# Kernel optimization log

Measured on AMD Instinct MI355X. Metric: run time of the kernel, lower is better.

## Reference

```python
import jax, jax.numpy as jnp
import numpy as np

EPS = 1e-8  # torch F.cosine_similarity default eps


def setup_inputs() -> dict:
    key = jax.random.key(0)
    k1, k2, k3 = jax.random.split(key, 3)
    B, S, D, O, W = 256, 10, 4096, 4096, 5
    x = jax.random.normal(k1, (B, S, D), dtype=jnp.float32)
    # Conv1d params: weight [out, in, kernel], bias [out]
    conv_w = jax.random.normal(k2, (O, D, W), dtype=jnp.float32) * (1.0 / np.sqrt(D * W))
    conv_b = jax.random.normal(k3, (O,), dtype=jnp.float32) * 0.01
    return {"x": x, "conv_w": conv_w, "conv_b": conv_b}


def reference(x, conv_w, conv_b):
    B, S, D = x.shape
    # central frame: original code uses index S//2 + 1 (faithful off-by-one)
    central = x[:, S // 2 + 1, :]  # [B, D]
    dots = jnp.einsum('bsd,bd->bs', x, central)  # [B, S]
    xn = jnp.maximum(jnp.linalg.norm(x, axis=-1), EPS)      # [B, S]
    cn = jnp.maximum(jnp.linalg.norm(central, axis=-1), EPS)  # [B]
    cos = dots / (xn * cn[:, None])  # [B, S]
    # original multiplies by RAW (unnormalized) cosine weights
    xw = x * cos[:, :, None]  # [B, S, D]
    # conv1d over time: [B, D, S] -> [B, O, S-W+1]
    y = jax.lax.conv_general_dilated(
        jnp.transpose(xw, (0, 2, 1)), conv_w,
        window_strides=(1,), padding='VALID',
        dimension_numbers=('NCH', 'OIH', 'NCH'))
    y = y + conv_b[None, :, None]
    return jnp.mean(y, axis=-1)  # [B, O]
```

## Files before the change

kernel.cpp:

```cpp
#include <hip/hip_runtime.h>


#define BDIM 256
#define SEQ 10
#define DDIM 4096
#define ODIM 4096
#define WDIM 5
#define GK 20480
#define SPLITS 8
#define KSPLIT (GK / SPLITS)
#define BK 64
#define KITERS (KSPLIT / BK)

typedef __bf16 bf16x8 __attribute__((ext_vector_type(8)));
typedef float f32x4 __attribute__((ext_vector_type(4)));

__device__ __forceinline__ unsigned short f2bf(float f) {
    union { float f; unsigned v; } c; c.f = f;
    unsigned r = c.v + 0x7FFFu + ((c.v >> 16) & 1u);
    return (unsigned short)(r >> 16);
}
__device__ __forceinline__ void async16(void* lds, const void* g) {
    __builtin_amdgcn_global_load_lds(
        (const __attribute__((address_space(1))) void*)g,
        (__attribute__((address_space(3))) void*)lds, 16, 0, 0);
}

#define VMWAIT(n) asm volatile("s_waitcnt vmcnt(" #n ")" ::: "memory")
#define LGKM0()   asm volatile("s_waitcnt lgkmcnt(0)" ::: "memory")
#define SBAR()    __builtin_amdgcn_s_barrier()
#define SCHED0()  __builtin_amdgcn_sched_barrier(0)

__global__ __launch_bounds__(256) void cosp_kernel(const float* __restrict__ x,
                                                   unsigned short* __restrict__ P)
{
    const int b = blockIdx.x;
    const int tid = threadIdx.x;
    const float* xb = x + (size_t)b * SEQ * DDIM;

    float dot[SEQ], sq[SEQ];
#pragma unroll
    for (int s = 0; s < SEQ; ++s) { dot[s] = 0.f; sq[s] = 0.f; }

    for (int base = 0; base < DDIM; base += 1024) {
        const int d = base + tid * 4;
        const f32x4 c4 = *(const f32x4*)(xb + 6 * DDIM + d);
#pragma unroll
        for (int s = 0; s < SEQ; ++s) {
            const f32x4 v4 = *(const f32x4*)(xb + s * DDIM + d);
            dot[s] += v4[0] * c4[0] + v4[1] * c4[1] + v4[2] * c4[2] + v4[3] * c4[3];
            sq[s]  += v4[0] * v4[0] + v4[1] * v4[1] + v4[2] * v4[2] + v4[3] * v4[3];
        }
    }
#pragma unroll
    for (int s = 0; s < SEQ; ++s) {
#pragma unroll
        for (int off = 32; off > 0; off >>= 1) {
            dot[s] += __shfl_down(dot[s], off, 64);
            sq[s]  += __shfl_down(sq[s], off, 64);
        }
    }
    __shared__ float red[4][2 * SEQ];
    __shared__ float cs[SEQ];
    const int wave = tid >> 6, lane = tid & 63;
    if (lane == 0) {
#pragma unroll
        for (int s = 0; s < SEQ; ++s) { red[wave][s] = dot[s]; red[wave][SEQ + s] = sq[s]; }
    }
    __syncthreads();
    if (tid == 0) {
        const float S6 = red[0][SEQ + 6] + red[1][SEQ + 6] + red[2][SEQ + 6] + red[3][SEQ + 6];
        const float cn = fmaxf(sqrtf(S6), 1e-8f);
#pragma unroll
        for (int s = 0; s < SEQ; ++s) {
            const float Dv = red[0][s] + red[1][s] + red[2][s] + red[3][s];
            const float Sv = red[0][SEQ + s] + red[1][SEQ + s] + red[2][SEQ + s] + red[3][SEQ + s];
            cs[s] = Dv / (fmaxf(sqrtf(Sv), 1e-8f) * cn);
        }
    }
    __syncthreads();

    float csr[SEQ];
#pragma unroll
    for (int s = 0; s < SEQ; ++s) csr[s] = cs[s];

    for (int chunk = 3; chunk >= 0; --chunk) {
        const int d0 = chunk * 1024 + tid * 4;
        const float* xd = xb + d0;
        float sc[SEQ][4];
#pragma unroll
        for (int s = 0; s < SEQ; ++s) {
            const f32x4 v4 = *(const f32x4*)(xd + s * DDIM);
            sc[s][0] = v4[0] * csr[s]; sc[s][1] = v4[1] * csr[s];
            sc[s][2] = v4[2] * csr[s]; sc[s][3] = v4[3] * csr[s];
        }
        __attribute__((aligned(16))) unsigned short o[20];
#pragma unroll
        for (int w = 0; w < WDIM; ++w) {
#pragma unroll
            for (int j = 0; j < 4; ++j) {
                const float p = sc[w][j] + sc[w + 1][j] + sc[w + 2][j] +
                                sc[w + 3][j] + sc[w + 4][j] + sc[w + 5][j];
                o[j * WDIM + w] = f2bf(p);
            }
        }
        unsigned short* dst = P + ((size_t)b * DDIM + d0) * WDIM;
#pragma unroll
        for (int q = 0; q < 5; ++q)
            *(uint2*)(dst + q * 4) = *(const uint2*)(o + q * 4);
    }
}

__global__ __launch_bounds__(256, 2) void gemm_splitk_kernel(const unsigned short* __restrict__ A,
                                                             const float* __restrict__ W,
                                                             float* __restrict__ Cpart)
{
    const int bid = blockIdx.x;
    const int sp = bid & 7;
    const int nt = bid >> 3;
    const int tid = threadIdx.x;
    const int lane = tid & 63;
    const int wave = tid >> 6;

    __shared__ __align__(16) unsigned short lds_a[2][256 * BK];
    __shared__ __align__(16) unsigned short lds_w[2][64 * BK];

    f32x4 acc[4][4];
#pragma unroll
    for (int i = 0; i < 4; ++i)
#pragma unroll
        for (int j = 0; j < 4; ++j)
            acc[i][j] = (f32x4){0.f, 0.f, 0.f, 0.f};

    const int s_arow = tid >> 3;
    const int s_aoct = tid & 7;

    const int s_wrow = tid >> 2;
    const float* wsrc = W + ((size_t)(nt * 64 + s_wrow)) * GK + (tid & 3) * 16;
    const int wo0 = (((tid & 3) * 2)     ^ (s_wrow & 7)) * 8;
    const int wo1 = (((tid & 3) * 2 + 1) ^ (s_wrow & 7)) * 8;

    const int fm = lane & 15;
    const int fg = lane >> 4;
    int aoff[2][4], woff[2][4];
#pragma unroll
    for (int i = 0; i < 4; ++i) {
        const int ra = wave * 64 + i * 16 + fm;
        const int rw = i * 16 + fm;
#pragma unroll
        for (int kh = 0; kh < 2; ++kh) {
            aoff[kh][i] = ra * BK + (((kh * 4 + fg) ^ (ra & 7)) * 8);
            woff[kh][i] = rw * BK + (((kh * 4 + fg) ^ (rw & 7)) * 8);
        }
    }

#define STAGE_A(buf, kk)                                                        \
    _Pragma("unroll")                                                           \
    for (int q = 0; q < 8; ++q) {                                               \
        const int row_ = q * 32 + s_arow;                                       \
        const unsigned short* src_ =                                            \
            A + (size_t)row_ * GK + (kk) + ((s_aoct ^ (row_ & 7)) * 8);         \
        async16((char*)&lds_a[buf][0] + q * 4096 + tid * 16, src_);             \
    }

#define LOAD_W(R0, R1, R2, R3, kk)                                              \
    R0 = *(const f32x4*)(wsrc + (kk));                                          \
    R1 = *(const f32x4*)(wsrc + (kk) + 4);                                      \
    R2 = *(const f32x4*)(wsrc + (kk) + 8);                                      \
    R3 = *(const f32x4*)(wsrc + (kk) + 12);

#define WRITE_W(buf, R0, R1, R2, R3)                                            \
    {                                                                           \
        bf16x8 lo_, hi_;                                                        \
        _Pragma("unroll")                                                       \
        for (int e = 0; e < 4; ++e) {                                           \
            lo_[e] = (__bf16)R0[e]; lo_[4 + e] = (__bf16)R1[e];                 \
            hi_[e] = (__bf16)R2[e]; hi_[4 + e] = (__bf16)R3[e];                 \
        }                                                                       \
        *(bf16x8*)&lds_w[buf][s_wrow * BK + wo0] = lo_;                         \
        *(bf16x8*)&lds_w[buf][s_wrow * BK + wo1] = hi_;                         \
    }

#define COMPUTE(buf)                                                            \
    _Pragma("unroll")                                                           \
    for (int kh = 0; kh < 2; ++kh) {                                            \
        bf16x8 af[4], wf[4];                                                    \
        _Pragma("unroll")                                                       \
        for (int i = 0; i < 4; ++i) af[i] = *(const bf16x8*)&lds_a[buf][aoff[kh][i]]; \
        _Pragma("unroll")                                                       \
        for (int j = 0; j < 4; ++j) wf[j] = *(const bf16x8*)&lds_w[buf][woff[kh][j]]; \
        _Pragma("unroll")                                                       \
        for (int i = 0; i < 4; ++i)                                             \
            _Pragma("unroll")                                                   \
            for (int j = 0; j < 4; ++j)                                         \
                acc[i][j] = __builtin_amdgcn_mfma_f32_16x16x32_bf16(            \
                    af[i], wf[j], acc[i][j], 0, 0, 0);                          \
    }

    const int ksp = sp * KSPLIT;
    f32x4 wA0, wA1, wA2, wA3;
    f32x4 wB0, wB1, wB2, wB3;

    LOAD_W(wA0, wA1, wA2, wA3, ksp);
    STAGE_A(0, ksp);
    VMWAIT(8); SCHED0();
    WRITE_W(0, wA0, wA1, wA2, wA3);
    LOAD_W(wB0, wB1, wB2, wB3, ksp + BK);
    VMWAIT(4); SCHED0();
    LGKM0();
    SBAR(); SCHED0();

    int kbase = ksp;
    for (int tt = 0; tt < (KITERS - 2) / 2; ++tt) {
        SCHED0();
        STAGE_A(1, kbase + BK);
        LOAD_W(wA0, wA1, wA2, wA3, kbase + 2 * BK);
        VMWAIT(12); SCHED0();
        COMPUTE(0);
        WRITE_W(1, wB0, wB1, wB2, wB3);
        LGKM0();
        SBAR(); SCHED0();
        kbase += BK;
        STAGE_A(0, kbase + BK);
        LOAD_W(wB0, wB1, wB2, wB3, kbase + 2 * BK);
        VMWAIT(12); SCHED0();
        COMPUTE(1);
        WRITE_W(0, wA0, wA1, wA2, wA3);
        LGKM0();
        SBAR(); SCHED0();
        kbase += BK;
    }
    STAGE_A(1, kbase + BK);
    VMWAIT(8); SCHED0();
    COMPUTE(0);
    WRITE_W(1, wB0, wB1, wB2, wB3);
    LGKM0();
    SBAR(); SCHED0();
    VMWAIT(0); SCHED0();
    COMPUTE(1);

    float* Cp = Cpart + (size_t)sp * (BDIM * ODIM);
    const int mbase = wave * 64 + fg * 4;
    const int nbase = nt * 64 + fm;
#pragma unroll
    for (int i = 0; i < 4; ++i)
#pragma unroll
        for (int j = 0; j < 4; ++j) {
            const int n = nbase + j * 16;
#pragma unroll
            for (int r = 0; r < 4; ++r) {
                const int m = mbase + i * 16 + r;
                Cp[(size_t)m * ODIM + n] = acc[i][j][r];
            }
        }
#undef STAGE_A
#undef LOAD_W
#undef WRITE_W
#undef COMPUTE
}

__global__ __launch_bounds__(256) void reduce_kernel(const float* __restrict__ part,
                                                     const float* __restrict__ bias,
                                                     float* __restrict__ out)
{
    const int idx = (blockIdx.x * 256 + threadIdx.x) * 4;
    f32x4 s = (f32x4){0.f, 0.f, 0.f, 0.f};
#pragma unroll
    for (int sp = 0; sp < SPLITS; ++sp) {
        const f32x4 v = *(const f32x4*)(part + (size_t)sp * (BDIM * ODIM) + idx);
        s[0] += v[0]; s[1] += v[1]; s[2] += v[2]; s[3] += v[3];
    }
    const int n = idx & (ODIM - 1);
    const f32x4 b4 = *(const f32x4*)(bias + n);
    const float inv6 = 1.0f / 6.0f;
    f32x4 o;
#pragma unroll
    for (int e = 0; e < 4; ++e) o[e] = s[e] * inv6 + b4[e];
    *(f32x4*)(out + idx) = o;
}

extern "C" void kernel_launch(void* const* d_in, const int* in_sizes, int n_in,
                              void* d_out, int out_size, void* d_ws, size_t ws_size,
                              hipStream_t stream) {
    const float* x  = (const float*)d_in[0];
    const float* cw = (const float*)d_in[1];
    const float* cb = (const float*)d_in[2];
    float* out = (float*)d_out;

    char* ws = (char*)d_ws;
    unsigned short* P = (unsigned short*)(ws + 16384);
    float* parts = (float*)(ws + 16384 + (size_t)BDIM * GK * 2);

    hipLaunchKernelGGL(cosp_kernel,        dim3(256),  dim3(256), 0, stream, x, P);
    hipLaunchKernelGGL(gemm_splitk_kernel, dim3(512),  dim3(256), 0, stream, P, cw, parts);
    hipLaunchKernelGGL(reduce_kernel,      dim3(1024), dim3(256), 0, stream, parts, cb, out);
}
```

Before: 493.3 us.

## Narrow GEMM N-tile to 32, halve split-K count, and move W waits after compute

Shrinks each block's output tile from 256x64 to 256x32 and cuts the split-K factor from 8 to 4, so the block count stays the same but each block covers twice the K range. Partial-sum writes and the final reduction shrink accordingly. W loads now move 8 floats per thread, and the vmcnt waits sit after the MFMA compute so W loads overlap with math. The narrower tile means the A operand is re-streamed by twice as many N-tiles. Each block also gets less MFMA work per LDS read, which may hurt arithmetic intensity.

```diff
diff --git a/kernel.cpp b/kernel.cpp
--- a/kernel.cpp
+++ b/kernel.cpp
@@ -7,10 +7,11 @@
 #define ODIM 4096
 #define WDIM 5
 #define GK 20480
-#define SPLITS 8
+#define SPLITS 4
 #define KSPLIT (GK / SPLITS)
 #define BK 64
 #define KITERS (KSPLIT / BK)
+#define NT 32
 
 typedef __bf16 bf16x8 __attribute__((ext_vector_type(8)));
 typedef float f32x4 __attribute__((ext_vector_type(4)));
@@ -116,41 +117,43 @@
                                                              float* __restrict__ Cpart)
 {
     const int bid = blockIdx.x;
-    const int sp = bid & 7;
-    const int nt = bid >> 3;
+    const int sp = bid & 3;
+    const int nt = bid >> 2;
     const int tid = threadIdx.x;
     const int lane = tid & 63;
     const int wave = tid >> 6;
 
     __shared__ __align__(16) unsigned short lds_a[2][256 * BK];
-    __shared__ __align__(16) unsigned short lds_w[2][64 * BK];
-
-    f32x4 acc[4][4];
+    __shared__ __align__(16) unsigned short lds_w[2][NT * BK];
+
+    f32x4 acc[4][2];
 #pragma unroll
     for (int i = 0; i < 4; ++i)
 #pragma unroll
-        for (int j = 0; j < 4; ++j)
+        for (int j = 0; j < 2; ++j)
             acc[i][j] = (f32x4){0.f, 0.f, 0.f, 0.f};
 
     const int s_arow = tid >> 3;
     const int s_aoct = tid & 7;
 
-    const int s_wrow = tid >> 2;
-    const float* wsrc = W + ((size_t)(nt * 64 + s_wrow)) * GK + (tid & 3) * 16;
-    const int wo0 = (((tid & 3) * 2)     ^ (s_wrow & 7)) * 8;
-    const int wo1 = (((tid & 3) * 2 + 1) ^ (s_wrow & 7)) * 8;
+    const int s_wrow = tid >> 3;
+    const float* wsrc = W + ((size_t)(nt * NT + s_wrow)) * GK + (tid & 7) * 8;
+    const int wo0 = (((tid & 7)) ^ (s_wrow & 7)) * 8;
 
     const int fm = lane & 15;
     const int fg = lane >> 4;
-    int aoff[2][4], woff[2][4];
-#pragma unroll
-    for (int i = 0; i < 4; ++i) {
-        const int ra = wave * 64 + i * 16 + fm;
-        const int rw = i * 16 + fm;
-#pragma unroll
-        for (int kh = 0; kh < 2; ++kh) {
+    int aoff[2][4], woff[2][2];
+#pragma unroll
+    for (int kh = 0; kh < 2; ++kh) {
+#pragma unroll
+        for (int i = 0; i < 4; ++i) {
+            const int ra = wave * 64 + i * 16 + fm;
             aoff[kh][i] = ra * BK + (((kh * 4 + fg) ^ (ra & 7)) * 8);
-            woff[kh][i] = rw * BK + (((kh * 4 + fg) ^ (rw & 7)) * 8);
+        }
+#pragma unroll
+        for (int j = 0; j < 2; ++j) {
+            const int rw = j * 16 + fm;
+            woff[kh][j] = rw * BK + (((kh * 4 + fg) ^ (rw & 7)) * 8);
         }
     }
 
@@ -163,50 +166,44 @@
         async16((char*)&lds_a[buf][0] + q * 4096 + tid * 16, src_);             \
     }
 
-#define LOAD_W(R0, R1, R2, R3, kk)                                              \
+#define LOAD_W(R0, R1, kk)                                                      \
     R0 = *(const f32x4*)(wsrc + (kk));                                          \
-    R1 = *(const f32x4*)(wsrc + (kk) + 4);                                      \
-    R2 = *(const f32x4*)(wsrc + (kk) + 8);                                      \
-    R3 = *(const f32x4*)(wsrc + (kk) + 12);
-
-#define WRITE_W(buf, R0, R1, R2, R3)                                            \
+    R1 = *(const f32x4*)(wsrc + (kk) + 4);
+
+#define WRITE_W(buf, R0, R1)                                                    \
     {                                                                           \
-        bf16x8 lo_, hi_;                                                        \
-        _Pragma("unroll")                                                       \
-        for (int e = 0; e < 4; ++e) {                                           \
-            lo_[e] = (__bf16)R0[e]; lo_[4 + e] = (__bf16)R1[e];                 \
-            hi_[e] = (__bf16)R2[e]; hi_[4 + e] = (__bf16)R3[e];                 \
-        }                                                                       \
-        *(bf16x8*)&lds_w[buf][s_wrow * BK + wo0] = lo_;                         \
-        *(bf16x8*)&lds_w[buf][s_wrow * BK + wo1] = hi_;                         \
+        bf16x8 v_;                                                              \
+        _Pragma("unroll")                                                       \
+        for (int e = 0; e < 4; ++e) { v_[e] = (__bf16)R0[e]; v_[4 + e] = (__bf16)R1[e]; } \
+        *(bf16x8*)&lds_w[buf][s_wrow * BK + wo0] = v_;                          \
     }
 
 #define COMPUTE(buf)                                                            \
     _Pragma("unroll")                                                           \
     for (int kh = 0; kh < 2; ++kh) {                                            \
-        bf16x8 af[4], wf[4];                                                    \
+        bf16x8 af[4], wf[2];                                                    \
         _Pragma("unroll")                                                       \
         for (int i = 0; i < 4; ++i) af[i] = *(const bf16x8*)&lds_a[buf][aoff[kh][i]]; \
         _Pragma("unroll")                                                       \
-        for (int j = 0; j < 4; ++j) wf[j] = *(const bf16x8*)&lds_w[buf][woff[kh][j]]; \
+        for (int j = 0; j < 2; ++j) wf[j] = *(const bf16x8*)&lds_w[buf][woff[kh][j]]; \
         _Pragma("unroll")                                                       \
         for (int i = 0; i < 4; ++i)                                             \
             _Pragma("unroll")                                                   \
-            for (int j = 0; j < 4; ++j)                                         \
+            for (int j = 0; j < 2; ++j)                                         \
                 acc[i][j] = __builtin_amdgcn_mfma_f32_16x16x32_bf16(            \
                     af[i], wf[j], acc[i][j], 0, 0, 0);                          \
     }
 
     const int ksp = sp * KSPLIT;
-    f32x4 wA0, wA1, wA2, wA3;
-    f32x4 wB0, wB1, wB2, wB3;
-
-    LOAD_W(wA0, wA1, wA2, wA3, ksp);
+    f32x4 wA0, wA1;
+    f32x4 wB0, wB1;
+
+    LOAD_W(wA0, wA1, ksp);
     STAGE_A(0, ksp);
-    VMWAIT(8); SCHED0();
-    WRITE_W(0, wA0, wA1, wA2, wA3);
-    LOAD_W(wB0, wB1, wB2, wB3, ksp + BK);
-    VMWAIT(4); SCHED0();
+    LOAD_W(wB0, wB1, ksp + BK);
+    VMWAIT(10); SCHED0();
+    WRITE_W(0, wA0, wA1);
+    VMWAIT(2); SCHED0();
     LGKM0();
     SBAR(); SCHED0();
 
@@ -214,38 +211,40 @@
     for (int tt = 0; tt < (KITERS - 2) / 2; ++tt) {
         SCHED0();
         STAGE_A(1, kbase + BK);
-        LOAD_W(wA0, wA1, wA2, wA3, kbase + 2 * BK);
-        VMWAIT(12); SCHED0();
+        LOAD_W(wA0, wA1, kbase + 2 * BK);
         COMPUTE(0);
-        WRITE_W(1, wB0, wB1, wB2, wB3);
+        VMWAIT(10); SCHED0();
+        WRITE_W(1, wB0, wB1);
+        VMWAIT(2); SCHED0();
         LGKM0();
         SBAR(); SCHED0();
         kbase += BK;
         STAGE_A(0, kbase + BK);
-        LOAD_W(wB0, wB1, wB2, wB3, kbase + 2 * BK);
-        VMWAIT(12); SCHED0();
+        LOAD_W(wB0, wB1, kbase + 2 * BK);
         COMPUTE(1);
-        WRITE_W(0, wA0, wA1, wA2, wA3);
+        VMWAIT(10); SCHED0();
+        WRITE_W(0, wA0, wA1);
+        VMWAIT(2); SCHED0();
         LGKM0();
         SBAR(); SCHED0();
         kbase += BK;
     }
     STAGE_A(1, kbase + BK);
+    COMPUTE(0);
     VMWAIT(8); SCHED0();
-    COMPUTE(0);
-    WRITE_W(1, wB0, wB1, wB2, wB3);
+    WRITE_W(1, wB0, wB1);
+    VMWAIT(0); SCHED0();
     LGKM0();
     SBAR(); SCHED0();
-    VMWAIT(0); SCHED0();
     COMPUTE(1);
 
     float* Cp = Cpart + (size_t)sp * (BDIM * ODIM);
     const int mbase = wave * 64 + fg * 4;
-    const int nbase = nt * 64 + fm;
+    const int nbase = nt * NT + fm;
 #pragma unroll
     for (int i = 0; i < 4; ++i)
 #pragma unroll
-        for (int j = 0; j < 4; ++j) {
+        for (int j = 0; j < 2; ++j) {
             const int n = nbase + j * 16;
 #pragma unroll
             for (int r = 0; r < 4; ++r) {
```

New measurement: 522.1 us. 5.8% more time.

## Store split-K partials as bf16 and overlap MFMA compute with pending loads

Applied to the files above, without the earlier changes.

Split-K partial sums are now written as bf16 instead of fp32, halving partial-buffer write and reduce read traffic; the reduce kernel handles 8 elements per thread with half the blocks. The GEMM pipeline is reordered so COMPUTE is issued before waiting on the in-flight W loads, and the second W prefetch is issued earlier in the prologue, aiming to hide global load latency behind MFMAs. Rounding partials to bf16 adds precision loss in the accumulated sums.

```diff
diff --git a/kernel.cpp b/kernel.cpp
--- a/kernel.cpp
+++ b/kernel.cpp
@@ -11,14 +11,20 @@
 #define KSPLIT (GK / SPLITS)
 #define BK 64
 #define KITERS (KSPLIT / BK)
+#define NT 64
 
 typedef __bf16 bf16x8 __attribute__((ext_vector_type(8)));
 typedef float f32x4 __attribute__((ext_vector_type(4)));
+typedef unsigned short u16x8 __attribute__((ext_vector_type(8)));
 
 __device__ __forceinline__ unsigned short f2bf(float f) {
     union { float f; unsigned v; } c; c.f = f;
     unsigned r = c.v + 0x7FFFu + ((c.v >> 16) & 1u);
     return (unsigned short)(r >> 16);
+}
+__device__ __forceinline__ float bf2f(unsigned short u) {
+    union { unsigned v; float f; } c; c.v = ((unsigned)u) << 16;
+    return c.f;
 }
 __device__ __forceinline__ void async16(void* lds, const void* g) {
     __builtin_amdgcn_global_load_lds(
@@ -113,7 +119,7 @@
 
 __global__ __launch_bounds__(256, 2) void gemm_splitk_kernel(const unsigned short* __restrict__ A,
                                                              const float* __restrict__ W,
-                                                             float* __restrict__ Cpart)
+                                                             unsigned short* __restrict__ Cpart)
 {
     const int bid = blockIdx.x;
     const int sp = bid & 7;
@@ -123,7 +129,7 @@
     const int wave = tid >> 6;
 
     __shared__ __align__(16) unsigned short lds_a[2][256 * BK];
-    __shared__ __align__(16) unsigned short lds_w[2][64 * BK];
+    __shared__ __align__(16) unsigned short lds_w[2][NT * BK];
 
     f32x4 acc[4][4];
 #pragma unroll
@@ -136,7 +142,7 @@
     const int s_aoct = tid & 7;
 
     const int s_wrow = tid >> 2;
-    const float* wsrc = W + ((size_t)(nt * 64 + s_wrow)) * GK + (tid & 3) * 16;
+    const float* wsrc = W + ((size_t)(nt * NT + s_wrow)) * GK + (tid & 3) * 16;
     const int wo0 = (((tid & 3) * 2)     ^ (s_wrow & 7)) * 8;
     const int wo1 = (((tid & 3) * 2 + 1) ^ (s_wrow & 7)) * 8;
 
@@ -144,13 +150,16 @@
     const int fg = lane >> 4;
     int aoff[2][4], woff[2][4];
 #pragma unroll
-    for (int i = 0; i < 4; ++i) {
-        const int ra = wave * 64 + i * 16 + fm;
-        const int rw = i * 16 + fm;
-#pragma unroll
-        for (int kh = 0; kh < 2; ++kh) {
+    for (int kh = 0; kh < 2; ++kh) {
+#pragma unroll
+        for (int i = 0; i < 4; ++i) {
+            const int ra = wave * 64 + i * 16 + fm;
             aoff[kh][i] = ra * BK + (((kh * 4 + fg) ^ (ra & 7)) * 8);
-            woff[kh][i] = rw * BK + (((kh * 4 + fg) ^ (rw & 7)) * 8);
+        }
+#pragma unroll
+        for (int j = 0; j < 4; ++j) {
+            const int rw = j * 16 + fm;
+            woff[kh][j] = rw * BK + (((kh * 4 + fg) ^ (rw & 7)) * 8);
         }
     }
 
@@ -203,9 +212,9 @@
 
     LOAD_W(wA0, wA1, wA2, wA3, ksp);
     STAGE_A(0, ksp);
+    LOAD_W(wB0, wB1, wB2, wB3, ksp + BK);
     VMWAIT(8); SCHED0();
     WRITE_W(0, wA0, wA1, wA2, wA3);
-    LOAD_W(wB0, wB1, wB2, wB3, ksp + BK);
     VMWAIT(4); SCHED0();
     LGKM0();
     SBAR(); SCHED0();
@@ -215,33 +224,35 @@
         SCHED0();
         STAGE_A(1, kbase + BK);
         LOAD_W(wA0, wA1, wA2, wA3, kbase + 2 * BK);
+        COMPUTE(0);
         VMWAIT(12); SCHED0();
-        COMPUTE(0);
         WRITE_W(1, wB0, wB1, wB2, wB3);
+        VMWAIT(4); SCHED0();
         LGKM0();
         SBAR(); SCHED0();
         kbase += BK;
         STAGE_A(0, kbase + BK);
         LOAD_W(wB0, wB1, wB2, wB3, kbase + 2 * BK);
+        COMPUTE(1);
         VMWAIT(12); SCHED0();
-        COMPUTE(1);
         WRITE_W(0, wA0, wA1, wA2, wA3);
+        VMWAIT(4); SCHED0();
         LGKM0();
         SBAR(); SCHED0();
         kbase += BK;
     }
     STAGE_A(1, kbase + BK);
+    COMPUTE(0);
     VMWAIT(8); SCHED0();
-    COMPUTE(0);
     WRITE_W(1, wB0, wB1, wB2, wB3);
+    VMWAIT(0); SCHED0();
     LGKM0();
     SBAR(); SCHED0();
-    VMWAIT(0); SCHED0();
     COMPUTE(1);
 
-    float* Cp = Cpart + (size_t)sp * (BDIM * ODIM);
+    unsigned short* Cp = Cpart + (size_t)sp * (BDIM * ODIM);
     const int mbase = wave * 64 + fg * 4;
-    const int nbase = nt * 64 + fm;
+    const int nbase = nt * NT + fm;
 #pragma unroll
     for (int i = 0; i < 4; ++i)
 #pragma unroll
@@ -250,7 +261,7 @@
 #pragma unroll
             for (int r = 0; r < 4; ++r) {
                 const int m = mbase + i * 16 + r;
-                Cp[(size_t)m * ODIM + n] = acc[i][j][r];
+                Cp[(size_t)m * ODIM + n] = f2bf(acc[i][j][r]);
             }
         }
 #undef STAGE_A
@@ -259,24 +270,30 @@
 #undef COMPUTE
 }
 
-__global__ __launch_bounds__(256) void reduce_kernel(const float* __restrict__ part,
+__global__ __launch_bounds__(256) void reduce_kernel(const unsigned short* __restrict__ part,
                                                      const float* __restrict__ bias,
                                                      float* __restrict__ out)
 {
-    const int idx = (blockIdx.x * 256 + threadIdx.x) * 4;
-    f32x4 s = (f32x4){0.f, 0.f, 0.f, 0.f};
+    const int idx = (blockIdx.x * 256 + threadIdx.x) * 8;
+    float s[8];
+#pragma unroll
+    for (int e = 0; e < 8; ++e) s[e] = 0.f;
 #pragma unroll
     for (int sp = 0; sp < SPLITS; ++sp) {
-        const f32x4 v = *(const f32x4*)(part + (size_t)sp * (BDIM * ODIM) + idx);
-        s[0] += v[0]; s[1] += v[1]; s[2] += v[2]; s[3] += v[3];
+        const u16x8 v = *(const u16x8*)(part + (size_t)sp * (BDIM * ODIM) + idx);
+#pragma unroll
+        for (int e = 0; e < 8; ++e) s[e] += bf2f(v[e]);
     }
     const int n = idx & (ODIM - 1);
-    const f32x4 b4 = *(const f32x4*)(bias + n);
     const float inv6 = 1.0f / 6.0f;
-    f32x4 o;
-#pragma unroll
-    for (int e = 0; e < 4; ++e) o[e] = s[e] * inv6 + b4[e];
-    *(f32x4*)(out + idx) = o;
+    f32x4 o0, o1;
+#pragma unroll
+    for (int e = 0; e < 4; ++e) {
+        o0[e] = s[e] * inv6 + bias[n + e];
+        o1[e] = s[4 + e] * inv6 + bias[n + 4 + e];
+    }
+    *(f32x4*)(out + idx) = o0;
+    *(f32x4*)(out + idx + 4) = o1;
 }
 
 extern "C" void kernel_launch(void* const* d_in, const int* in_sizes, int n_in,
@@ -289,9 +306,9 @@
 
     char* ws = (char*)d_ws;
     unsigned short* P = (unsigned short*)(ws + 16384);
-    float* parts = (float*)(ws + 16384 + (size_t)BDIM * GK * 2);
+    unsigned short* parts = (unsigned short*)(ws + 16384 + (size_t)BDIM * GK * 2);
 
     hipLaunchKernelGGL(cosp_kernel,        dim3(256),  dim3(256), 0, stream, x, P);
     hipLaunchKernelGGL(gemm_splitk_kernel, dim3(512),  dim3(256), 0, stream, P, cw, parts);
-    hipLaunchKernelGGL(reduce_kernel,      dim3(1024), dim3(256), 0, stream, parts, cb, out);
-}
+    hipLaunchKernelGGL(reduce_kernel,      dim3(512),  dim3(256), 0, stream, parts, cb, out);
+}
```

After: 492.7 us. Within noise of the previous version (-0.1%).
